# Performance work log

Hardware: AMD Instinct MI355X
Metric: run time of the kernel (lower is better)

## Reference

```python
import jax, jax.numpy as jnp
import numpy as np
import math

B, L, D = 4, 2048, 768
N_HEADS = 12
CHUNK = 8  # query_mask=1 every CHUNK tokens -> f = B*L/CHUNK, f % B == 0
VOCAB = 50000


def setup_inputs() -> dict:
    key = jax.random.key(0)
    ks = jax.random.split(key, 8)
    scale = 1.0 / math.sqrt(D)
    x_qk = jax.random.normal(ks[0], (B, L, D), jnp.float32)
    x_v = jax.random.normal(ks[1], (B, L, D), jnp.float32)
    # deterministic query mask: feature boundary every CHUNK tokens
    pos = jnp.arange(L)
    query_mask = jnp.tile((pos % CHUNK == 0).astype(jnp.int32)[None, :], (B, 1))
    input_ids = jax.random.randint(ks[2], (B, L), 2, VOCAB).astype(jnp.int64)
    # make the last 16 tokens of each row padding to exercise the pad mask
    input_ids = input_ids.at[:, -16:].set(1)
    Wq = jax.random.normal(ks[3], (D, D), jnp.float32) * scale
    Wk = jax.random.normal(ks[4], (D, D), jnp.float32) * scale
    Wv = jax.random.normal(ks[5], (D, D), jnp.float32) * scale
    Wo = jax.random.normal(ks[6], (D, D), jnp.float32) * scale
    zb = jnp.zeros((D,), jnp.float32)
    return {"x_qk": x_qk, "x_v": x_v, "query_mask": query_mask,
            "input_ids": input_ids, "pad_token_id": 1,
            "Wq": Wq, "bq": zb, "Wk": Wk, "bk": zb,
            "Wv": Wv, "bv": zb, "Wo": Wo, "bo": zb}


def reference(x_qk, x_v, query_mask, input_ids, pad_token_id,
              Wq, bq, Wk, bk, Wv, bv, Wo, bo):
    b, l, d = x_qk.shape
    n = b * l
    qm = query_mask.reshape(-1)
    f = int(np.asarray(jnp.sum(qm)))  # static feature count (f % b == 0)
    idx = jnp.nonzero(qm == 1, size=f)[0]                     # [f] query positions
    # segment boundaries: [left_i, right_i) per feature
    left = idx
    right = jnp.concatenate([idx[1:], jnp.array([n], idx.dtype)])
    pos = jnp.arange(n)
    seg_mask = (pos[None, :] >= left[:, None]) & (pos[None, :] < right[:, None])
    seg_mask = seg_mask & (input_ids.reshape(-1) != pad_token_id)[None, :]  # [f, n]

    xq = x_qk.reshape(n, d)
    xv = x_v.reshape(n, d)
    query = xq[idx]                                           # [f, d]
    q = query @ Wq.T + bq                                     # [f, d]
    k = xq @ Wk.T + bk                                        # [n, d]
    v = xv @ Wv.T + bv                                        # [n, d]

    dh = d // N_HEADS
    qh = q.reshape(f, N_HEADS, dh).transpose(1, 0, 2)         # [h, f, dh]
    kh = k.reshape(n, N_HEADS, dh).transpose(1, 0, 2)         # [h, n, dh]
    vh = v.reshape(n, N_HEADS, dh).transpose(1, 0, 2)         # [h, n, dh]

    bias = (1.0 - seg_mask.astype(jnp.float32)) * -10000.0    # [f, n]
    scores = jnp.einsum('hfd,hnd->hfn', qh, kh) / math.sqrt(dh) + bias[None]
    attn = jax.nn.softmax(scores, axis=-1)                    # [h, f, n]
    out = jnp.einsum('hfn,hnd->hfd', attn, vh)                # [h, f, dh]
    out = out.transpose(1, 0, 2).reshape(f, d)
    out = out @ Wo.T + bo
    return out.reshape(b, f // b, d)
```

## Files before the change

### kernel.cpp

```cpp
#include <hip/hip_runtime.h>

#define DMODEL 768
#define NHEADS 12
#define MAXFULL 16
#define NSTEP 24

typedef __attribute__((ext_vector_type(8))) short short8;
typedef __attribute__((ext_vector_type(4))) float f32x4;

__device__ __forceinline__ unsigned pack2_bf16(float a, float b) {
  unsigned ua = __float_as_uint(a), ub = __float_as_uint(b);
  ua = (ua + 0x7fffu + ((ua >> 16) & 1u)) >> 16;
  ub = (ub + 0x7fffu + ((ub >> 16) & 1u)) & 0xffff0000u;
  return ua | ub;
}
__device__ __forceinline__ unsigned short bf16_1(float a) {
  unsigned ua = __float_as_uint(a);
  return (unsigned short)((ua + 0x7fffu + ((ua >> 16) & 1u)) >> 16);
}

__device__ __forceinline__ void load16_lds(const void* g, void* l) {
  __builtin_amdgcn_global_load_lds(
      (const __attribute__((address_space(1))) unsigned int*)g,
      (__attribute__((address_space(3))) unsigned int*)l, 16, 0, 0);
}

__global__ __launch_bounds__(256) void convAll(const float* __restrict__ w0,
    const float* __restrict__ w1, const float* __restrict__ w2,
    const float* __restrict__ w3, unsigned* __restrict__ o0,
    unsigned* __restrict__ o1, unsigned* __restrict__ o2,
    unsigned* __restrict__ o3, int wcount,
    const float* __restrict__ x0, const float* __restrict__ x1,
    unsigned* __restrict__ xo0, unsigned* __restrict__ xo1, int xcount) {
  const int nvw = wcount >> 2;
  const float* src[4] = {w0, w1, w2, w3};
  unsigned* dst[4] = {o0, o1, o2, o3};
  for (int idx = blockIdx.x * 256 + threadIdx.x; idx < 4 * nvw;
       idx += gridDim.x * 256) {
    int m = idx / nvw, r = idx - m * nvw;
    float4 v = ((const float4*)src[m])[r];
    dst[m][2 * r]     = pack2_bf16(v.x, v.y);
    dst[m][2 * r + 1] = pack2_bf16(v.z, v.w);
  }
  const int nvx = xcount >> 2;
  for (int idx = blockIdx.x * 256 + threadIdx.x; idx < 2 * nvx;
       idx += gridDim.x * 256) {
    int m = idx / nvx, r = idx - m * nvx;
    float4 v = m ? ((const float4*)x1)[r] : ((const float4*)x0)[r];
    unsigned* d = m ? xo1 : xo0;
    d[2 * r]     = pack2_bf16(v.x, v.y);
    d[2 * r + 1] = pack2_bf16(v.z, v.w);
  }
}

struct GSeg {
  const unsigned short* A;
  const unsigned short* W;
  const float* bias;
  const int* row_map;
  float* C;
  int base;
};

typedef unsigned short LdsTile[2][256][32];

__global__ __launch_bounds__(512, 2) void gemm256(GSeg g0, GSeg g1, GSeg g2) {
  __shared__ __attribute__((aligned(16))) LdsTile As[2];
  __shared__ __attribute__((aligned(16))) LdsTile Bs[2];
  const int t = threadIdx.x;
  const int id = blockIdx.x;
  const GSeg& d = (id >= g2.base) ? g2 : ((id >= g1.base) ? g1 : g0);
  const int lid = id - d.base;
  const int bn = (lid % 3) * 256;
  const int bm = (lid / 3) * 256;
  const int lane = t & 63, wid = t >> 6;
  const int m16 = lane & 15, quad = lane >> 4;
  const int qx = quad ^ ((m16 >> 1) & 3);
  const int wr = wid >> 2, wc = wid & 3;

  f32x4 acc[8][4];
#pragma unroll
  for (int i = 0; i < 8; ++i)
#pragma unroll
    for (int j2 = 0; j2 < 4; ++j2) acc[i][j2] = (f32x4){0.f, 0.f, 0.f, 0.f};

  const int srow = wid * 16 + (lane >> 2);
  const int skc = ((lane & 3) ^ ((lane >> 3) & 3)) * 8;
  int arow0, arow1;
  if (d.row_map) {
    arow0 = d.row_map[bm + srow];
    arow1 = d.row_map[bm + 128 + srow];
  } else {
    arow0 = bm + srow;
    arow1 = bm + 128 + srow;
  }
  const int wrow0 = bn + srow, wrow1 = bn + 128 + srow;
  const int woff0 = (wid * 16) * 32;
  const int woff1 = (128 + wid * 16) * 32;

#define STAGE256(t_, Ab, Bb) do {                                          \
    const int kk_ = (t_) * 64 + skc;                                       \
    load16_lds(d.A + (size_t)arow0 * DMODEL + kk_,      &Ab[0][0][0] + woff0); \
    load16_lds(d.A + (size_t)arow1 * DMODEL + kk_,      &Ab[0][0][0] + woff1); \
    load16_lds(d.A + (size_t)arow0 * DMODEL + kk_ + 32, &Ab[1][0][0] + woff0); \
    load16_lds(d.A + (size_t)arow1 * DMODEL + kk_ + 32, &Ab[1][0][0] + woff1); \
    load16_lds(d.W + (size_t)wrow0 * DMODEL + kk_,      &Bb[0][0][0] + woff0); \
    load16_lds(d.W + (size_t)wrow1 * DMODEL + kk_,      &Bb[0][0][0] + woff1); \
    load16_lds(d.W + (size_t)wrow0 * DMODEL + kk_ + 32, &Bb[1][0][0] + woff0); \
    load16_lds(d.W + (size_t)wrow1 * DMODEL + kk_ + 32, &Bb[1][0][0] + woff1); \
  } while (0)

#define COMPUTE256(Ab, Bb) do {                                            \
    _Pragma("unroll")                                                      \
    for (int ks = 0; ks < 2; ++ks) {                                       \
      const unsigned short* Ap = &Ab[ks][0][0];                            \
      const unsigned short* Bp = &Bb[ks][0][0];                            \
      short8 a_[8], b_[4];                                                 \
      _Pragma("unroll")                                                    \
      for (int mi = 0; mi < 8; ++mi)                                       \
        a_[mi] = *(const short8*)&Ap[(wr * 128 + mi * 16 + m16) * 32 + qx * 8]; \
      _Pragma("unroll")                                                    \
      for (int nj = 0; nj < 4; ++nj)                                       \
        b_[nj] = *(const short8*)&Bp[(wc * 64 + nj * 16 + m16) * 32 + qx * 8]; \
      __builtin_amdgcn_s_setprio(1);                                       \
      _Pragma("unroll")                                                    \
      for (int mi = 0; mi < 8; ++mi)                                       \
        _Pragma("unroll")                                                  \
        for (int nj = 0; nj < 4; ++nj)                                     \
          acc[mi][nj] = __builtin_amdgcn_mfma_f32_16x16x32_bf16(           \
              a_[mi], b_[nj], acc[mi][nj], 0, 0, 0);                       \
      __builtin_amdgcn_s_setprio(0);                                       \
    }                                                                      \
  } while (0)

  STAGE256(0, As[0], Bs[0]);
  STAGE256(1, As[1], Bs[1]);

#pragma unroll 1
  for (int g = 0; g < 5; ++g) {
    asm volatile("s_waitcnt vmcnt(8)" ::: "memory");
    __builtin_amdgcn_s_barrier();
    __builtin_amdgcn_sched_barrier(0);
    COMPUTE256(As[0], Bs[0]);
    __builtin_amdgcn_s_barrier();
    __builtin_amdgcn_sched_barrier(0);
    STAGE256(2 * g + 2, As[0], Bs[0]);
    asm volatile("s_waitcnt vmcnt(8)" ::: "memory");
    __builtin_amdgcn_s_barrier();
    __builtin_amdgcn_sched_barrier(0);
    COMPUTE256(As[1], Bs[1]);
    __builtin_amdgcn_s_barrier();
    __builtin_amdgcn_sched_barrier(0);
    STAGE256(2 * g + 3, As[1], Bs[1]);
  }
  asm volatile("s_waitcnt vmcnt(8)" ::: "memory");
  __builtin_amdgcn_s_barrier();
  __builtin_amdgcn_sched_barrier(0);
  COMPUTE256(As[0], Bs[0]);
  asm volatile("s_waitcnt vmcnt(0)" ::: "memory");
  __builtin_amdgcn_s_barrier();
  __builtin_amdgcn_sched_barrier(0);
  COMPUTE256(As[1], Bs[1]);

#undef STAGE256
#undef COMPUTE256

  float bv[4]; int bcol[4];
#pragma unroll
  for (int nj = 0; nj < 4; ++nj) {
    bcol[nj] = bn + wc * 64 + nj * 16 + m16;
    bv[nj] = d.bias[bcol[nj]];
  }
#pragma unroll
  for (int mi = 0; mi < 8; ++mi) {
    const int rbase = bm + wr * 128 + mi * 16 + quad * 4;
#pragma unroll
    for (int r = 0; r < 4; ++r) {
      const int row = rbase + r;
#pragma unroll
      for (int nj = 0; nj < 4; ++nj)
        d.C[(size_t)row * DMODEL + bcol[nj]] = acc[mi][nj][r] + bv[nj];
    }
  }
}

__device__ __forceinline__ void stage_step(const GSeg& d, int k0, int arow0,
    int arow1, int wrow0, int wrow1, int skc, unsigned short* AsB,
    unsigned short* BsB, int woff) {
  load16_lds(d.A + (size_t)arow0 * DMODEL + k0 + skc, AsB + woff);
  load16_lds(d.A + (size_t)arow1 * DMODEL + k0 + skc, AsB + woff + 16 * 32);
  load16_lds(d.W + (size_t)wrow0 * DMODEL + k0 + skc, BsB + woff);
  load16_lds(d.W + (size_t)wrow1 * DMODEL + k0 + skc, BsB + woff + 16 * 32);
}

__device__ __forceinline__ void compute_step(const unsigned short* AsB,
    const unsigned short* BsB, int wm, int wn, int m16, int qx,
    f32x4 acc[4][4]) {
  short8 a[4], b[4];
#pragma unroll
  for (int i = 0; i < 4; ++i)
    a[i] = *(const short8*)&AsB[(wm + i * 16 + m16) * 32 + qx * 8];
#pragma unroll
  for (int j2 = 0; j2 < 4; ++j2)
    b[j2] = *(const short8*)&BsB[(wn + j2 * 16 + m16) * 32 + qx * 8];
  __builtin_amdgcn_s_setprio(1);
#pragma unroll
  for (int i = 0; i < 4; ++i)
#pragma unroll
    for (int j2 = 0; j2 < 4; ++j2)
      acc[i][j2] = __builtin_amdgcn_mfma_f32_16x16x32_bf16(a[i], b[j2], acc[i][j2], 0, 0, 0);
  __builtin_amdgcn_s_setprio(0);
}

__global__ __launch_bounds__(256) void gemm128(GSeg g0, GSeg g1, GSeg g2) {
  __shared__ __attribute__((aligned(16))) unsigned short As[3][128 * 32];
  __shared__ __attribute__((aligned(16))) unsigned short Bs[3][128 * 32];
  const int t = threadIdx.x;
  const int id = blockIdx.x;
  const GSeg& d = (id >= g2.base) ? g2 : ((id >= g1.base) ? g1 : g0);
  const int lid = id - d.base;
  const int xcd = lid & 7, j = lid >> 3;
  const int bn = (j % 6) * 128;
  const int bm = ((j / 6) * 8 + xcd) * 128;
  const int lane = t & 63, wid = t >> 6;
  const int m16 = lane & 15, quad = lane >> 4;
  const int qx = quad ^ ((m16 >> 1) & 3);
  const int wm = (wid >> 1) * 64, wn = (wid & 1) * 64;

  f32x4 acc[4][4];
#pragma unroll
  for (int i = 0; i < 4; ++i)
#pragma unroll
    for (int j2 = 0; j2 < 4; ++j2) acc[i][j2] = (f32x4){0.f, 0.f, 0.f, 0.f};

  const int srow = wid * 32 + (lane >> 2);
  const int skc = ((lane & 3) ^ ((lane >> 3) & 3)) * 8;
  int arow0, arow1;
  if (d.row_map) {
    arow0 = d.row_map[bm + srow];
    arow1 = d.row_map[bm + srow + 16];
  } else {
    arow0 = bm + srow;
    arow1 = bm + srow + 16;
  }
  const int wrow0 = bn + srow, wrow1 = bn + srow + 16;
  const int woff = (wid * 32) * 32;

  stage_step(d, 0,  arow0, arow1, wrow0, wrow1, skc, &As[0][0], &Bs[0][0], woff);
  stage_step(d, 32, arow0, arow1, wrow0, wrow1, skc, &As[1][0], &Bs[1][0], woff);
  stage_step(d, 64, arow0, arow1, wrow0, wrow1, skc, &As[2][0], &Bs[2][0], woff);

#pragma unroll 1
  for (int g = 0; g < (NSTEP - 3) / 3; ++g) {
    const int t0 = g * 3;
#pragma unroll
    for (int u = 0; u < 3; ++u) {
      const int ts = t0 + u;
      asm volatile("s_waitcnt vmcnt(8)" ::: "memory");
      __builtin_amdgcn_s_barrier();
      __builtin_amdgcn_sched_barrier(0);
      compute_step(&As[u][0], &Bs[u][0], wm, wn, m16, qx, acc);
      __builtin_amdgcn_s_barrier();
      __builtin_amdgcn_sched_barrier(0);
      stage_step(d, (ts + 3) * 32, arow0, arow1, wrow0, wrow1, skc,
                 &As[u][0], &Bs[u][0], woff);
    }
  }
  asm volatile("s_waitcnt vmcnt(8)" ::: "memory");
  __builtin_amdgcn_s_barrier();
  __builtin_amdgcn_sched_barrier(0);
  compute_step(&As[0][0], &Bs[0][0], wm, wn, m16, qx, acc);
  asm volatile("s_waitcnt vmcnt(4)" ::: "memory");
  __builtin_amdgcn_s_barrier();
  __builtin_amdgcn_sched_barrier(0);
  compute_step(&As[1][0], &Bs[1][0], wm, wn, m16, qx, acc);
  asm volatile("s_waitcnt vmcnt(0)" ::: "memory");
  __builtin_amdgcn_s_barrier();
  __builtin_amdgcn_sched_barrier(0);
  compute_step(&As[2][0], &Bs[2][0], wm, wn, m16, qx, acc);

  float bv[4]; int bcol[4];
#pragma unroll
  for (int j2 = 0; j2 < 4; ++j2) {
    bcol[j2] = bn + wn + j2 * 16 + m16;
    bv[j2] = d.bias[bcol[j2]];
  }
#pragma unroll
  for (int i = 0; i < 4; ++i) {
    const int rbase = bm + wm + i * 16 + quad * 4;
#pragma unroll
    for (int r = 0; r < 4; ++r) {
      const int row = rbase + r;
#pragma unroll
      for (int j2 = 0; j2 < 4; ++j2)
        d.C[(size_t)row * DMODEL + bcol[j2]] = acc[i][j2][r] + bv[j2];
    }
  }
}

__global__ __launch_bounds__(1024) void build_segments(const int* __restrict__ qm,
    const int* __restrict__ ids, const int* __restrict__ padp,
    int n, int f, int* __restrict__ left, int* __restrict__ right,
    int* __restrict__ nvalid, int* __restrict__ fullrank,
    int* __restrict__ fullist, int* __restrict__ nfull) {
  __shared__ int cnt[1024];
  __shared__ int fullcnt;
  const int t = threadIdx.x;
  if (t == 0) fullcnt = 0;
  const int per = (n + 1023) >> 10;
  const int base = t * per;
  int c = 0;
  for (int i = 0; i < per; ++i) {
    int p = base + i;
    if (p < n && qm[p] != 0) ++c;
  }
  cnt[t] = c;
  __syncthreads();
  for (int off = 1; off < 1024; off <<= 1) {
    int v = (t >= off) ? cnt[t - off] : 0;
    __syncthreads();
    cnt[t] += v;
    __syncthreads();
  }
  int r = cnt[t] - c;
  for (int i = 0; i < per; ++i) {
    int p = base + i;
    if (p < n && qm[p] != 0) {
      if (r < f) left[r] = p;
      ++r;
    }
  }
  __syncthreads();
  const int pad = *padp;
  for (int i = t; i < f; i += 1024) {
    int L0 = left[i];
    int R0 = (i + 1 < f) ? left[i + 1] : n;
    right[i] = R0;
    int cv = 0;
    for (int p = L0; p < R0; ++p) cv += (ids[p] != pad) ? 1 : 0;
    nvalid[i] = cv;
    if (cv == 0) {
      int rk = atomicAdd(&fullcnt, 1);
      if (rk < MAXFULL) { fullist[rk] = i; fullrank[i] = rk; }
      else fullrank[i] = -1;
    } else {
      fullrank[i] = -1;
    }
  }
  __syncthreads();
  if (t == 0) *nfull = (fullcnt < MAXFULL) ? fullcnt : MAXFULL;
}

__device__ __forceinline__ float allreduce64(float x) {
#pragma unroll
  for (int m = 1; m < 64; m <<= 1) x += __shfl_xor(x, m, 64);
  return x;
}

__global__ __launch_bounds__(64) void attn_seg(const float* __restrict__ q,
    const float* __restrict__ k, const float* __restrict__ v,
    const int* __restrict__ left, const int* __restrict__ right,
    const int* __restrict__ nvalid, const int* __restrict__ ids,
    const int* __restrict__ padp, unsigned short* __restrict__ out) {
  const int feat = blockIdx.x, h = blockIdx.y, lane = threadIdx.x;
  if (nvalid[feat] == 0) return;
  const int off = h * 64 + lane;
  const int pad = *padp;
  const float qv = q[(size_t)feat * DMODEL + off];
  const int L0 = left[feat], R0 = right[feat];
  if (R0 - L0 == 8) {
    float kv[8], vv[8], s[8];
    int live[8];
#pragma unroll
    for (int p = 0; p < 8; ++p) {
      kv[p] = k[(size_t)(L0 + p) * DMODEL + off];
      vv[p] = v[(size_t)(L0 + p) * DMODEL + off];
      live[p] = (ids[L0 + p] != pad);
    }
#pragma unroll
    for (int p = 0; p < 8; ++p) s[p] = qv * kv[p];
#pragma unroll
    for (int m_ = 1; m_ < 64; m_ <<= 1)
#pragma unroll
      for (int p = 0; p < 8; ++p) s[p] += __shfl_xor(s[p], m_, 64);
    float mx = -1e30f;
#pragma unroll
    for (int p = 0; p < 8; ++p) {
      s[p] = live[p] ? s[p] * 0.125f : -1e30f;
      mx = fmaxf(mx, s[p]);
    }
    float l = 0.f, acc = 0.f;
#pragma unroll
    for (int p = 0; p < 8; ++p) {
      float w = __expf(s[p] - mx);
      l += w;
      acc += w * vv[p];
    }
    out[(size_t)feat * DMODEL + off] = bf16_1(acc / l);
    return;
  }
  float m = -1e30f, l = 0.f, acc = 0.f;
  for (int p = L0; p < R0; ++p) {
    if (ids[p] == pad) continue;
    float s = allreduce64(qv * k[(size_t)p * DMODEL + off]) * 0.125f;
    float mn = fmaxf(m, s);
    float al = __expf(m - mn);
    float w = __expf(s - mn);
    l = l * al + w;
    acc = acc * al + w * v[(size_t)p * DMODEL + off];
    m = mn;
  }
  out[(size_t)feat * DMODEL + off] = bf16_1(acc / l);
}

__global__ __launch_bounds__(256) void attn_full_part(const float* __restrict__ q,
    const float* __restrict__ k, const float* __restrict__ v,
    const int* __restrict__ fullist, const int* __restrict__ nfullp,
    int n, int P, float* __restrict__ pm, float* __restrict__ pl,
    float* __restrict__ pacc) {
  const int nfull = *nfullp;
  if (nfull == 0) return;
  const int t = threadIdx.x, lane = t & 63, wv = t >> 6;
  const int gw = blockIdx.x * 4 + wv;
  const int h = gw / P, piece = gw - h * P;
  const int pk = n / P;

  __shared__ float q_lds[8 * 64];
  __shared__ float w_lds[4][64 * 8];

  for (int idx = t; idx < 8 * 64; idx += 256) {
    int fl = idx >> 6, d = idx & 63;
    q_lds[idx] = (fl < nfull) ? q[(size_t)fullist[fl] * DMODEL + h * 64 + d] : 0.f;
  }
  __syncthreads();

  float m[8], l[8], acc[8];
#pragma unroll
  for (int f_ = 0; f_ < 8; ++f_) { m[f_] = -1e30f; l[f_] = 0.f; acc[f_] = 0.f; }

  for (int c = 0; c < pk; c += 64) {
    const int pc = piece * pk + c;
    float s[8];
#pragma unroll
    for (int f_ = 0; f_ < 8; ++f_) s[f_] = 0.f;
    const float4* kp = (const float4*)(k + (size_t)(pc + lane) * DMODEL + h * 64);
#pragma unroll 1
    for (int g = 0; g < 2; ++g) {
      float4 kv0 = kp[g * 8 + 0], kv1 = kp[g * 8 + 1], kv2 = kp[g * 8 + 2],
             kv3 = kp[g * 8 + 3], kv4 = kp[g * 8 + 4], kv5 = kp[g * 8 + 5],
             kv6 = kp[g * 8 + 6], kv7 = kp[g * 8 + 7];
      const float4* qb = (const float4*)&q_lds[g * 32];
#pragma unroll
      for (int f_ = 0; f_ < 8; ++f_) {
        float4 q0 = qb[f_ * 16 + 0], q1 = qb[f_ * 16 + 1], q2 = qb[f_ * 16 + 2],
               q3 = qb[f_ * 16 + 3], q4 = qb[f_ * 16 + 4], q5 = qb[f_ * 16 + 5],
               q6 = qb[f_ * 16 + 6], q7 = qb[f_ * 16 + 7];
        float acc0 = q0.x * kv0.x + q0.y * kv0.y + q0.z * kv0.z + q0.w * kv0.w;
        acc0 += q1.x * kv1.x + q1.y * kv1.y + q1.z * kv1.z + q1.w * kv1.w;
        acc0 += q2.x * kv2.x + q2.y * kv2.y + q2.z * kv2.z + q2.w * kv2.w;
        acc0 += q3.x * kv3.x + q3.y * kv3.y + q3.z * kv3.z + q3.w * kv3.w;
        acc0 += q4.x * kv4.x + q4.y * kv4.y + q4.z * kv4.z + q4.w * kv4.w;
        acc0 += q5.x * kv5.x + q5.y * kv5.y + q5.z * kv5.z + q5.w * kv5.w;
        acc0 += q6.x * kv6.x + q6.y * kv6.y + q6.z * kv6.z + q6.w * kv6.w;
        acc0 += q7.x * kv7.x + q7.y * kv7.y + q7.z * kv7.z + q7.w * kv7.w;
        s[f_] += acc0;
      }
    }
    float mx[8];
#pragma unroll
    for (int f_ = 0; f_ < 8; ++f_) mx[f_] = s[f_] * 0.125f;
#pragma unroll
    for (int f_ = 0; f_ < 8; ++f_) s[f_] = mx[f_];
#pragma unroll
    for (int st = 1; st < 64; st <<= 1)
#pragma unroll
      for (int f_ = 0; f_ < 8; ++f_) mx[f_] = fmaxf(mx[f_], __shfl_xor(mx[f_], st, 64));
    float alpha[8], w[8], sum[8];
#pragma unroll
    for (int f_ = 0; f_ < 8; ++f_) {
      float mn = fmaxf(m[f_], mx[f_]);
      alpha[f_] = __expf(m[f_] - mn);
      w[f_] = __expf(s[f_] - mn);
      m[f_] = mn;
      sum[f_] = w[f_];
    }
#pragma unroll
    for (int st = 1; st < 64; st <<= 1)
#pragma unroll
      for (int f_ = 0; f_ < 8; ++f_) sum[f_] += __shfl_xor(sum[f_], st, 64);
#pragma unroll
    for (int f_ = 0; f_ < 8; ++f_) l[f_] = l[f_] * alpha[f_] + sum[f_];
    *(float4*)&w_lds[wv][lane * 8]     = make_float4(w[0], w[1], w[2], w[3]);
    *(float4*)&w_lds[wv][lane * 8 + 4] = make_float4(w[4], w[5], w[6], w[7]);
#pragma unroll
    for (int f_ = 0; f_ < 8; ++f_) acc[f_] *= alpha[f_];
    const float* vb = v + (size_t)pc * DMODEL + h * 64 + lane;
#pragma unroll 4
    for (int kk = 0; kk < 64; ++kk) {
      float vd = vb[(size_t)kk * DMODEL];
      float4 wa = *(const float4*)&w_lds[wv][kk * 8];
      float4 wb = *(const float4*)&w_lds[wv][kk * 8 + 4];
      acc[0] += wa.x * vd; acc[1] += wa.y * vd; acc[2] += wa.z * vd; acc[3] += wa.w * vd;
      acc[4] += wb.x * vd; acc[5] += wb.y * vd; acc[6] += wb.z * vd; acc[7] += wb.w * vd;
    }
  }

  for (int f_ = 0; f_ < nfull; ++f_) {
    size_t idx = ((size_t)f_ * NHEADS + h) * P + piece;
    if (lane == 0) { pm[idx] = m[f_]; pl[idx] = l[f_]; }
    pacc[idx * 64 + lane] = acc[f_];
  }
}

__global__ __launch_bounds__(256) void attn_full_comb(
    const int* __restrict__ fullist, const int* __restrict__ nfullp,
    int P, const float* __restrict__ pm, const float* __restrict__ pl,
    const float* __restrict__ pacc, unsigned short* __restrict__ out) {
  const int fl = blockIdx.x, h = blockIdx.y;
  if (fl >= *nfullp) return;
  const int feat = fullist[fl];
  const int t = threadIdx.x, lane = t & 63, wv = t >> 6;
  const size_t base = ((size_t)fl * NHEADS + h) * P;

  __shared__ float s_pm[128];
  __shared__ float s_sc[128];
  __shared__ float s_red[4];
  __shared__ float s_part[4][64];

  for (int sp = t; sp < P; sp += 256) s_pm[sp] = pm[base + sp];
  __syncthreads();
  float mloc = -1e30f;
  for (int sp = t; sp < P; sp += 256) mloc = fmaxf(mloc, s_pm[sp]);
#pragma unroll
  for (int st = 1; st < 64; st <<= 1) mloc = fmaxf(mloc, __shfl_xor(mloc, st, 64));
  if (lane == 0) s_red[wv] = mloc;
  __syncthreads();
  const float M = fmaxf(fmaxf(s_red[0], s_red[1]), fmaxf(s_red[2], s_red[3]));
  __syncthreads();
  float lloc = 0.f;
  for (int sp = t; sp < P; sp += 256) {
    float sc = __expf(s_pm[sp] - M);
    s_sc[sp] = sc;
    lloc += pl[base + sp] * sc;
  }
#pragma unroll
  for (int st = 1; st < 64; st <<= 1) lloc += __shfl_xor(lloc, st, 64);
  if (lane == 0) s_red[wv] = lloc;
  __syncthreads();
  const float Lt = s_red[0] + s_red[1] + s_red[2] + s_red[3];
  float At = 0.f;
  for (int sp = wv; sp < P; sp += 4)
    At += pacc[(base + sp) * 64 + lane] * s_sc[sp];
  s_part[wv][lane] = At;
  __syncthreads();
  if (wv == 0) {
    float tot = s_part[0][lane] + s_part[1][lane] + s_part[2][lane] + s_part[3][lane];
    out[(size_t)feat * DMODEL + h * 64 + lane] = bf16_1(tot / Lt);
  }
}

extern "C" void kernel_launch(void* const* d_in, const int* in_sizes, int n_in,
                              void* d_out, int out_size, void* d_ws, size_t ws_size,
                              hipStream_t stream) {
  const float* x_qk = (const float*)d_in[0];
  const float* x_v  = (const float*)d_in[1];
  const int* qm     = (const int*)d_in[2];
  const int* ids    = (const int*)d_in[3];
  const int* padp   = (const int*)d_in[4];
  const float* Wq = (const float*)d_in[5];
  const float* bq = (const float*)d_in[6];
  const float* Wk = (const float*)d_in[7];
  const float* bk = (const float*)d_in[8];
  const float* Wv = (const float*)d_in[9];
  const float* bv = (const float*)d_in[10];
  const float* Wo = (const float*)d_in[11];
  const float* bo = (const float*)d_in[12];

  const int n = in_sizes[0] / DMODEL;
  const int f = out_size / DMODEL;

  float* kf = (float*)d_ws;
  float* vf = kf + (size_t)n * DMODEL;
  float* qf = vf + (size_t)n * DMODEL;
  unsigned short* af = (unsigned short*)(qf + (size_t)f * DMODEL);
  unsigned short* wqb = af + (size_t)f * DMODEL;
  unsigned short* wkb = wqb + DMODEL * DMODEL;
  unsigned short* wvb = wkb + DMODEL * DMODEL;
  unsigned short* wob = wvb + DMODEL * DMODEL;
  unsigned short* xqb = wob + DMODEL * DMODEL;
  unsigned short* xvb = xqb + (size_t)n * DMODEL;
  int* left     = (int*)(xvb + (size_t)n * DMODEL);
  int* right    = left + f;
  int* nvalid   = right + f;
  int* fullrank = nvalid + f;
  int* fullist  = fullrank + f;
  int* nfull    = fullist + MAXFULL;
  size_t off_bytes = ((size_t)((char*)(nfull + 1) - (char*)d_ws) + 255) & ~(size_t)255;
  int P = 128;
  while (P > 16) {
    size_t need = (size_t)MAXFULL * NHEADS * P * 66 * sizeof(float);
    if (off_bytes + need <= ws_size && (n / P) % 64 == 0 && n % P == 0) break;
    P >>= 1;
  }
  float* pm = (float*)((char*)d_ws + off_bytes);
  float* pl = pm + (size_t)MAXFULL * NHEADS * P;
  float* pacc = pl + (size_t)MAXFULL * NHEADS * P;

  build_segments<<<1, 1024, 0, stream>>>(qm, ids, padp, n, f, left, right,
                                         nvalid, fullrank, fullist, nfull);
  convAll<<<2048, 256, 0, stream>>>(Wq, Wk, Wv, Wo, (unsigned*)wqb,
                                    (unsigned*)wkb, (unsigned*)wvb,
                                    (unsigned*)wob, DMODEL * DMODEL,
                                    x_qk, x_v, (unsigned*)xqb, (unsigned*)xvb,
                                    n * DMODEL);

  const int TKV256 = 3 * (n / 256);
  const int TF256  = 3 * (f / 256);
  GSeg g0 = { xqb, wkb, bk, nullptr, kf, 0 };
  GSeg g1 = { xvb, wvb, bv, nullptr, vf, TKV256 };
  GSeg g2 = { xqb, wqb, bq, left,    qf, 2 * TKV256 };
  gemm256<<<2 * TKV256 + TF256, 512, 0, stream>>>(g0, g1, g2);

  attn_seg<<<dim3(f, NHEADS), 64, 0, stream>>>(qf, kf, vf, left, right, nvalid,
                                               ids, padp, af);
  attn_full_part<<<NHEADS * P / 4, 256, 0, stream>>>(qf, kf, vf, fullist, nfull,
                                                     n, P, pm, pl, pacc);
  attn_full_comb<<<dim3(MAXFULL, NHEADS), 256, 0, stream>>>(fullist, nfull, P,
                                                            pm, pl, pacc, af);

  const int TF  = 6 * (f / 128);
  GSeg gout = { af, wob, bo, nullptr, (float*)d_out, 0 };
  GSeg gnull = { af, wob, bo, nullptr, (float*)d_out, 1 << 30 };
  gemm128<<<TF, 256, 0, stream>>>(gout, gnull, gnull);
}
```

Baseline: 219.2 us.

## Fuse segment building into conversion, merge attention kernels, smaller-tile Wo GEMM

Folds the single-block build_segments launch into the extra last block of the conversion kernel, merges the segment-attention and full-attention-partial kernels into one launch, and replaces the 128x128 four-wave output GEMM with a single-wave 64x64 kernel that uses a 4-stage load pipeline and no barriers. The goal is fewer kernel launches and more blocks for the small f x 768 output GEMM (f=1024). The risk is that the segment-building block now runs with 256 threads instead of 1024 and may become the critical path of the conversion kernel, and single-wave GEMM blocks are less efficient per CU.

After: 223.5 us. No clear change (+2.0%).

```diff
diff --git a/kernel.cpp b/kernel.cpp
--- a/kernel.cpp
+++ b/kernel.cpp
@@ -31,20 +31,73 @@
     unsigned* __restrict__ o1, unsigned* __restrict__ o2,
     unsigned* __restrict__ o3, int wcount,
     const float* __restrict__ x0, const float* __restrict__ x1,
-    unsigned* __restrict__ xo0, unsigned* __restrict__ xo1, int xcount) {
+    unsigned* __restrict__ xo0, unsigned* __restrict__ xo1, int xcount,
+    const int* __restrict__ qm, const int* __restrict__ ids,
+    const int* __restrict__ padp, int n, int f, int* __restrict__ left,
+    int* __restrict__ right, int* __restrict__ nvalid,
+    int* __restrict__ fullrank, int* __restrict__ fullist,
+    int* __restrict__ nfull) {
+  __shared__ int cnt[256];
+  __shared__ int fullcnt;
+  const int t = threadIdx.x;
+  if (blockIdx.x == gridDim.x - 1) {
+    if (t == 0) fullcnt = 0;
+    const int per = (n + 255) >> 8;
+    const int base = t * per;
+    int c = 0;
+    for (int i = 0; i < per; ++i) {
+      int p = base + i;
+      if (p < n && qm[p] != 0) ++c;
+    }
+    cnt[t] = c;
+    __syncthreads();
+    for (int off = 1; off < 256; off <<= 1) {
+      int v = (t >= off) ? cnt[t - off] : 0;
+      __syncthreads();
+      cnt[t] += v;
+      __syncthreads();
+    }
+    int r = cnt[t] - c;
+    for (int i = 0; i < per; ++i) {
+      int p = base + i;
+      if (p < n && qm[p] != 0) {
+        if (r < f) left[r] = p;
+        ++r;
+      }
+    }
+    __syncthreads();
+    const int pad = *padp;
+    for (int i = t; i < f; i += 256) {
+      int L0 = left[i];
+      int R0 = (i + 1 < f) ? left[i + 1] : n;
+      right[i] = R0;
+      int cv = 0;
+      for (int p = L0; p < R0; ++p) cv += (ids[p] != pad) ? 1 : 0;
+      nvalid[i] = cv;
+      if (cv == 0) {
+        int rk = atomicAdd(&fullcnt, 1);
+        if (rk < MAXFULL) { fullist[rk] = i; fullrank[i] = rk; }
+        else fullrank[i] = -1;
+      } else {
+        fullrank[i] = -1;
+      }
+    }
+    __syncthreads();
+    if (t == 0) *nfull = (fullcnt < MAXFULL) ? fullcnt : MAXFULL;
+    return;
+  }
+  const int nb = gridDim.x - 1;
   const int nvw = wcount >> 2;
   const float* src[4] = {w0, w1, w2, w3};
   unsigned* dst[4] = {o0, o1, o2, o3};
-  for (int idx = blockIdx.x * 256 + threadIdx.x; idx < 4 * nvw;
-       idx += gridDim.x * 256) {
+  for (int idx = blockIdx.x * 256 + t; idx < 4 * nvw; idx += nb * 256) {
     int m = idx / nvw, r = idx - m * nvw;
     float4 v = ((const float4*)src[m])[r];
     dst[m][2 * r]     = pack2_bf16(v.x, v.y);
     dst[m][2 * r + 1] = pack2_bf16(v.z, v.w);
   }
   const int nvx = xcount >> 2;
-  for (int idx = blockIdx.x * 256 + threadIdx.x; idx < 2 * nvx;
-       idx += gridDim.x * 256) {
+  for (int idx = blockIdx.x * 256 + t; idx < 2 * nvx; idx += nb * 256) {
     int m = idx / nvx, r = idx - m * nvx;
     float4 v = m ? ((const float4*)x1)[r] : ((const float4*)x0)[r];
     unsigned* d = m ? xo1 : xo0;
@@ -184,48 +237,18 @@
   }
 }
 
-__device__ __forceinline__ void stage_step(const GSeg& d, int k0, int arow0,
-    int arow1, int wrow0, int wrow1, int skc, unsigned short* AsB,
-    unsigned short* BsB, int woff) {
-  load16_lds(d.A + (size_t)arow0 * DMODEL + k0 + skc, AsB + woff);
-  load16_lds(d.A + (size_t)arow1 * DMODEL + k0 + skc, AsB + woff + 16 * 32);
-  load16_lds(d.W + (size_t)wrow0 * DMODEL + k0 + skc, BsB + woff);
-  load16_lds(d.W + (size_t)wrow1 * DMODEL + k0 + skc, BsB + woff + 16 * 32);
-}
-
-__device__ __forceinline__ void compute_step(const unsigned short* AsB,
-    const unsigned short* BsB, int wm, int wn, int m16, int qx,
-    f32x4 acc[4][4]) {
-  short8 a[4], b[4];
-#pragma unroll
-  for (int i = 0; i < 4; ++i)
-    a[i] = *(const short8*)&AsB[(wm + i * 16 + m16) * 32 + qx * 8];
-#pragma unroll
-  for (int j2 = 0; j2 < 4; ++j2)
-    b[j2] = *(const short8*)&BsB[(wn + j2 * 16 + m16) * 32 + qx * 8];
-  __builtin_amdgcn_s_setprio(1);
-#pragma unroll
-  for (int i = 0; i < 4; ++i)
-#pragma unroll
-    for (int j2 = 0; j2 < 4; ++j2)
-      acc[i][j2] = __builtin_amdgcn_mfma_f32_16x16x32_bf16(a[i], b[j2], acc[i][j2], 0, 0, 0);
-  __builtin_amdgcn_s_setprio(0);
-}
-
-__global__ __launch_bounds__(256) void gemm128(GSeg g0, GSeg g1, GSeg g2) {
-  __shared__ __attribute__((aligned(16))) unsigned short As[3][128 * 32];
-  __shared__ __attribute__((aligned(16))) unsigned short Bs[3][128 * 32];
-  const int t = threadIdx.x;
-  const int id = blockIdx.x;
-  const GSeg& d = (id >= g2.base) ? g2 : ((id >= g1.base) ? g1 : g0);
-  const int lid = id - d.base;
-  const int xcd = lid & 7, j = lid >> 3;
-  const int bn = (j % 6) * 128;
-  const int bm = ((j / 6) * 8 + xcd) * 128;
-  const int lane = t & 63, wid = t >> 6;
+__global__ __launch_bounds__(64) void gemmWo(const unsigned short* __restrict__ A,
+    const unsigned short* __restrict__ W, const float* __restrict__ bias,
+    float* __restrict__ C) {
+  __shared__ __attribute__((aligned(16))) unsigned short As[4][64 * 32];
+  __shared__ __attribute__((aligned(16))) unsigned short Bs[4][64 * 32];
+  const int bid = blockIdx.x;
+  const int bm = (bid / 12) * 64, bn = (bid % 12) * 64;
+  const int lane = threadIdx.x;
   const int m16 = lane & 15, quad = lane >> 4;
   const int qx = quad ^ ((m16 >> 1) & 3);
-  const int wm = (wid >> 1) * 64, wn = (wid & 1) * 64;
+  const int srow = lane >> 2;
+  const int skc = ((lane & 3) ^ ((lane >> 3) & 3)) * 8;
 
   f32x4 acc[4][4];
 #pragma unroll
@@ -233,122 +256,77 @@
 #pragma unroll
     for (int j2 = 0; j2 < 4; ++j2) acc[i][j2] = (f32x4){0.f, 0.f, 0.f, 0.f};
 
-  const int srow = wid * 32 + (lane >> 2);
-  const int skc = ((lane & 3) ^ ((lane >> 3) & 3)) * 8;
-  int arow0, arow1;
-  if (d.row_map) {
-    arow0 = d.row_map[bm + srow];
-    arow1 = d.row_map[bm + srow + 16];
-  } else {
-    arow0 = bm + srow;
-    arow1 = bm + srow + 16;
-  }
-  const int wrow0 = bn + srow, wrow1 = bn + srow + 16;
-  const int woff = (wid * 32) * 32;
-
-  stage_step(d, 0,  arow0, arow1, wrow0, wrow1, skc, &As[0][0], &Bs[0][0], woff);
-  stage_step(d, 32, arow0, arow1, wrow0, wrow1, skc, &As[1][0], &Bs[1][0], woff);
-  stage_step(d, 64, arow0, arow1, wrow0, wrow1, skc, &As[2][0], &Bs[2][0], woff);
+#define STAGEW(s_, t_) do {                                                \
+    const int kk_ = (t_) * 32 + skc;                                       \
+    _Pragma("unroll")                                                      \
+    for (int i_ = 0; i_ < 4; ++i_) {                                       \
+      load16_lds(A + (size_t)(bm + 16 * i_ + srow) * DMODEL + kk_,         \
+                 &As[s_][i_ * 16 * 32]);                                   \
+      load16_lds(W + (size_t)(bn + 16 * i_ + srow) * DMODEL + kk_,         \
+                 &Bs[s_][i_ * 16 * 32]);                                   \
+    }                                                                      \
+  } while (0)
+
+#define COMPUTEW(s_) do {                                                  \
+    short8 a_[4], b_[4];                                                   \
+    _Pragma("unroll")                                                      \
+    for (int mi = 0; mi < 4; ++mi)                                         \
+      a_[mi] = *(const short8*)&As[s_][(mi * 16 + m16) * 32 + qx * 8];     \
+    _Pragma("unroll")                                                      \
+    for (int nj = 0; nj < 4; ++nj)                                         \
+      b_[nj] = *(const short8*)&Bs[s_][(nj * 16 + m16) * 32 + qx * 8];     \
+    _Pragma("unroll")                                                      \
+    for (int mi = 0; mi < 4; ++mi)                                         \
+      _Pragma("unroll")                                                    \
+      for (int nj = 0; nj < 4; ++nj)                                       \
+        acc[mi][nj] = __builtin_amdgcn_mfma_f32_16x16x32_bf16(             \
+            a_[mi], b_[nj], acc[mi][nj], 0, 0, 0);                         \
+  } while (0)
+
+  STAGEW(0, 0); STAGEW(1, 1); STAGEW(2, 2); STAGEW(3, 3);
 
 #pragma unroll 1
-  for (int g = 0; g < (NSTEP - 3) / 3; ++g) {
-    const int t0 = g * 3;
-#pragma unroll
-    for (int u = 0; u < 3; ++u) {
-      const int ts = t0 + u;
-      asm volatile("s_waitcnt vmcnt(8)" ::: "memory");
-      __builtin_amdgcn_s_barrier();
-      __builtin_amdgcn_sched_barrier(0);
-      compute_step(&As[u][0], &Bs[u][0], wm, wn, m16, qx, acc);
-      __builtin_amdgcn_s_barrier();
-      __builtin_amdgcn_sched_barrier(0);
-      stage_step(d, (ts + 3) * 32, arow0, arow1, wrow0, wrow1, skc,
-                 &As[u][0], &Bs[u][0], woff);
-    }
-  }
+  for (int ts = 0; ts < NSTEP - 4; ++ts) {
+    asm volatile("s_waitcnt vmcnt(24)" ::: "memory");
+    __builtin_amdgcn_sched_barrier(0);
+    COMPUTEW(ts & 3);
+    asm volatile("s_waitcnt lgkmcnt(0)" ::: "memory");
+    __builtin_amdgcn_sched_barrier(0);
+    STAGEW(ts & 3, ts + 4);
+  }
+  asm volatile("s_waitcnt vmcnt(24)" ::: "memory");
+  __builtin_amdgcn_sched_barrier(0);
+  COMPUTEW(0);
+  asm volatile("s_waitcnt vmcnt(16)" ::: "memory");
+  __builtin_amdgcn_sched_barrier(0);
+  COMPUTEW(1);
   asm volatile("s_waitcnt vmcnt(8)" ::: "memory");
-  __builtin_amdgcn_s_barrier();
   __builtin_amdgcn_sched_barrier(0);
-  compute_step(&As[0][0], &Bs[0][0], wm, wn, m16, qx, acc);
-  asm volatile("s_waitcnt vmcnt(4)" ::: "memory");
-  __builtin_amdgcn_s_barrier();
+  COMPUTEW(2);
+  asm volatile("s_waitcnt vmcnt(0)" ::: "memory");
   __builtin_amdgcn_sched_barrier(0);
-  compute_step(&As[1][0], &Bs[1][0], wm, wn, m16, qx, acc);
-  asm volatile("s_waitcnt vmcnt(0)" ::: "memory");
-  __builtin_amdgcn_s_barrier();
-  __builtin_amdgcn_sched_barrier(0);
-  compute_step(&As[2][0], &Bs[2][0], wm, wn, m16, qx, acc);
+  COMPUTEW(3);
+
+#undef STAGEW
+#undef COMPUTEW
 
   float bv[4]; int bcol[4];
 #pragma unroll
-  for (int j2 = 0; j2 < 4; ++j2) {
-    bcol[j2] = bn + wn + j2 * 16 + m16;
-    bv[j2] = d.bias[bcol[j2]];
-  }
-#pragma unroll
-  for (int i = 0; i < 4; ++i) {
-    const int rbase = bm + wm + i * 16 + quad * 4;
+  for (int nj = 0; nj < 4; ++nj) {
+    bcol[nj] = bn + nj * 16 + m16;
+    bv[nj] = bias[bcol[nj]];
+  }
+#pragma unroll
+  for (int mi = 0; mi < 4; ++mi) {
+    const int rbase = bm + mi * 16 + quad * 4;
 #pragma unroll
     for (int r = 0; r < 4; ++r) {
       const int row = rbase + r;
 #pragma unroll
-      for (int j2 = 0; j2 < 4; ++j2)
-        d.C[(size_t)row * DMODEL + bcol[j2]] = acc[i][j2][r] + bv[j2];
-    }
-  }
-}
-
-__global__ __launch_bounds__(1024) void build_segments(const int* __restrict__ qm,
-    const int* __restrict__ ids, const int* __restrict__ padp,
-    int n, int f, int* __restrict__ left, int* __restrict__ right,
-    int* __restrict__ nvalid, int* __restrict__ fullrank,
-    int* __restrict__ fullist, int* __restrict__ nfull) {
-  __shared__ int cnt[1024];
-  __shared__ int fullcnt;
-  const int t = threadIdx.x;
-  if (t == 0) fullcnt = 0;
-  const int per = (n + 1023) >> 10;
-  const int base = t * per;
-  int c = 0;
-  for (int i = 0; i < per; ++i) {
-    int p = base + i;
-    if (p < n && qm[p] != 0) ++c;
-  }
-  cnt[t] = c;
-  __syncthreads();
-  for (int off = 1; off < 1024; off <<= 1) {
-    int v = (t >= off) ? cnt[t - off] : 0;
-    __syncthreads();
-    cnt[t] += v;
-    __syncthreads();
-  }
-  int r = cnt[t] - c;
-  for (int i = 0; i < per; ++i) {
-    int p = base + i;
-    if (p < n && qm[p] != 0) {
-      if (r < f) left[r] = p;
-      ++r;
-    }
-  }
-  __syncthreads();
-  const int pad = *padp;
-  for (int i = t; i < f; i += 1024) {
-    int L0 = left[i];
-    int R0 = (i + 1 < f) ? left[i + 1] : n;
-    right[i] = R0;
-    int cv = 0;
-    for (int p = L0; p < R0; ++p) cv += (ids[p] != pad) ? 1 : 0;
-    nvalid[i] = cv;
-    if (cv == 0) {
-      int rk = atomicAdd(&fullcnt, 1);
-      if (rk < MAXFULL) { fullist[rk] = i; fullrank[i] = rk; }
-      else fullrank[i] = -1;
-    } else {
-      fullrank[i] = -1;
-    }
-  }
-  __syncthreads();
-  if (t == 0) *nfull = (fullcnt < MAXFULL) ? fullcnt : MAXFULL;
+      for (int nj = 0; nj < 4; ++nj)
+        C[(size_t)row * DMODEL + bcol[nj]] = acc[mi][nj][r] + bv[nj];
+    }
+  }
 }
 
 __device__ __forceinline__ float allreduce64(float x) {
@@ -357,80 +335,79 @@
   return x;
 }
 
-__global__ __launch_bounds__(64) void attn_seg(const float* __restrict__ q,
+__global__ __launch_bounds__(64) void attn_all(const float* __restrict__ q,
     const float* __restrict__ k, const float* __restrict__ v,
     const int* __restrict__ left, const int* __restrict__ right,
     const int* __restrict__ nvalid, const int* __restrict__ ids,
-    const int* __restrict__ padp, unsigned short* __restrict__ out) {
-  const int feat = blockIdx.x, h = blockIdx.y, lane = threadIdx.x;
-  if (nvalid[feat] == 0) return;
-  const int off = h * 64 + lane;
-  const int pad = *padp;
-  const float qv = q[(size_t)feat * DMODEL + off];
-  const int L0 = left[feat], R0 = right[feat];
-  if (R0 - L0 == 8) {
-    float kv[8], vv[8], s[8];
-    int live[8];
-#pragma unroll
-    for (int p = 0; p < 8; ++p) {
-      kv[p] = k[(size_t)(L0 + p) * DMODEL + off];
-      vv[p] = v[(size_t)(L0 + p) * DMODEL + off];
-      live[p] = (ids[L0 + p] != pad);
-    }
-#pragma unroll
-    for (int p = 0; p < 8; ++p) s[p] = qv * kv[p];
-#pragma unroll
-    for (int m_ = 1; m_ < 64; m_ <<= 1)
-#pragma unroll
-      for (int p = 0; p < 8; ++p) s[p] += __shfl_xor(s[p], m_, 64);
-    float mx = -1e30f;
-#pragma unroll
-    for (int p = 0; p < 8; ++p) {
-      s[p] = live[p] ? s[p] * 0.125f : -1e30f;
-      mx = fmaxf(mx, s[p]);
-    }
-    float l = 0.f, acc = 0.f;
-#pragma unroll
-    for (int p = 0; p < 8; ++p) {
-      float w = __expf(s[p] - mx);
-      l += w;
-      acc += w * vv[p];
+    const int* __restrict__ padp, unsigned short* __restrict__ out,
+    const int* __restrict__ fullist, const int* __restrict__ nfullp,
+    int n, int f, int P, float* __restrict__ pm, float* __restrict__ pl,
+    float* __restrict__ pacc) {
+  __shared__ float q_lds[8 * 64];
+  __shared__ float w_lds[64 * 8];
+  const int x = blockIdx.x, h = blockIdx.y, lane = threadIdx.x;
+
+  if (x < f) {
+    const int feat = x;
+    if (nvalid[feat] == 0) return;
+    const int off = h * 64 + lane;
+    const int pad = *padp;
+    const float qv = q[(size_t)feat * DMODEL + off];
+    const int L0 = left[feat], R0 = right[feat];
+    if (R0 - L0 == 8) {
+      float kv[8], vv[8], s[8];
+      int live[8];
+#pragma unroll
+      for (int p = 0; p < 8; ++p) {
+        kv[p] = k[(size_t)(L0 + p) * DMODEL + off];
+        vv[p] = v[(size_t)(L0 + p) * DMODEL + off];
+        live[p] = (ids[L0 + p] != pad);
+      }
+#pragma unroll
+      for (int p = 0; p < 8; ++p) s[p] = qv * kv[p];
+#pragma unroll
+      for (int m_ = 1; m_ < 64; m_ <<= 1)
+#pragma unroll
+        for (int p = 0; p < 8; ++p) s[p] += __shfl_xor(s[p], m_, 64);
+      float mx = -1e30f;
+#pragma unroll
+      for (int p = 0; p < 8; ++p) {
+        s[p] = live[p] ? s[p] * 0.125f : -1e30f;
+        mx = fmaxf(mx, s[p]);
+      }
+      float l = 0.f, acc = 0.f;
+#pragma unroll
+      for (int p = 0; p < 8; ++p) {
+        float w = __expf(s[p] - mx);
+        l += w;
+        acc += w * vv[p];
+      }
+      out[(size_t)feat * DMODEL + off] = bf16_1(acc / l);
+      return;
+    }
+    float m = -1e30f, l = 0.f, acc = 0.f;
+    for (int p = L0; p < R0; ++p) {
+      if (ids[p] == pad) continue;
+      float s = allreduce64(qv * k[(size_t)p * DMODEL + off]) * 0.125f;
+      float mn = fmaxf(m, s);
+      float al = __expf(m - mn);
+      float w = __expf(s - mn);
+      l = l * al + w;
+      acc = acc * al + w * v[(size_t)p * DMODEL + off];
+      m = mn;
     }
     out[(size_t)feat * DMODEL + off] = bf16_1(acc / l);
     return;
   }
-  float m = -1e30f, l = 0.f, acc = 0.f;
-  for (int p = L0; p < R0; ++p) {
-    if (ids[p] == pad) continue;
-    float s = allreduce64(qv * k[(size_t)p * DMODEL + off]) * 0.125f;
-    float mn = fmaxf(m, s);
-    float al = __expf(m - mn);
-    float w = __expf(s - mn);
-    l = l * al + w;
-    acc = acc * al + w * v[(size_t)p * DMODEL + off];
-    m = mn;
-  }
-  out[(size_t)feat * DMODEL + off] = bf16_1(acc / l);
-}
-
-__global__ __launch_bounds__(256) void attn_full_part(const float* __restrict__ q,
-    const float* __restrict__ k, const float* __restrict__ v,
-    const int* __restrict__ fullist, const int* __restrict__ nfullp,
-    int n, int P, float* __restrict__ pm, float* __restrict__ pl,
-    float* __restrict__ pacc) {
+
   const int nfull = *nfullp;
   if (nfull == 0) return;
-  const int t = threadIdx.x, lane = t & 63, wv = t >> 6;
-  const int gw = blockIdx.x * 4 + wv;
-  const int h = gw / P, piece = gw - h * P;
+  const int piece = x - f;
   const int pk = n / P;
 
-  __shared__ float q_lds[8 * 64];
-  __shared__ float w_lds[4][64 * 8];
-
-  for (int idx = t; idx < 8 * 64; idx += 256) {
-    int fl = idx >> 6, d = idx & 63;
-    q_lds[idx] = (fl < nfull) ? q[(size_t)fullist[fl] * DMODEL + h * 64 + d] : 0.f;
+  for (int idx = lane; idx < 8 * 64; idx += 64) {
+    int fl = idx >> 6, dcol = idx & 63;
+    q_lds[idx] = (fl < nfull) ? q[(size_t)fullist[fl] * DMODEL + h * 64 + dcol] : 0.f;
   }
   __syncthreads();
 
@@ -490,16 +467,16 @@
       for (int f_ = 0; f_ < 8; ++f_) sum[f_] += __shfl_xor(sum[f_], st, 64);
 #pragma unroll
     for (int f_ = 0; f_ < 8; ++f_) l[f_] = l[f_] * alpha[f_] + sum[f_];
-    *(float4*)&w_lds[wv][lane * 8]     = make_float4(w[0], w[1], w[2], w[3]);
-    *(float4*)&w_lds[wv][lane * 8 + 4] = make_float4(w[4], w[5], w[6], w[7]);
+    *(float4*)&w_lds[lane * 8]     = make_float4(w[0], w[1], w[2], w[3]);
+    *(float4*)&w_lds[lane * 8 + 4] = make_float4(w[4], w[5], w[6], w[7]);
 #pragma unroll
     for (int f_ = 0; f_ < 8; ++f_) acc[f_] *= alpha[f_];
     const float* vb = v + (size_t)pc * DMODEL + h * 64 + lane;
 #pragma unroll 4
     for (int kk = 0; kk < 64; ++kk) {
       float vd = vb[(size_t)kk * DMODEL];
-      float4 wa = *(const float4*)&w_lds[wv][kk * 8];
-      float4 wb = *(const float4*)&w_lds[wv][kk * 8 + 4];
+      float4 wa = *(const float4*)&w_lds[kk * 8];
+      float4 wb = *(const float4*)&w_lds[kk * 8 + 4];
       acc[0] += wa.x * vd; acc[1] += wa.y * vd; acc[2] += wa.z * vd; acc[3] += wa.w * vd;
       acc[4] += wb.x * vd; acc[5] += wb.y * vd; acc[6] += wb.z * vd; acc[7] += wb.w * vd;
     }
@@ -606,13 +583,13 @@
   float* pl = pm + (size_t)MAXFULL * NHEADS * P;
   float* pacc = pl + (size_t)MAXFULL * NHEADS * P;
 
-  build_segments<<<1, 1024, 0, stream>>>(qm, ids, padp, n, f, left, right,
-                                         nvalid, fullrank, fullist, nfull);
-  convAll<<<2048, 256, 0, stream>>>(Wq, Wk, Wv, Wo, (unsigned*)wqb,
+  convAll<<<2049, 256, 0, stream>>>(Wq, Wk, Wv, Wo, (unsigned*)wqb,
                                     (unsigned*)wkb, (unsigned*)wvb,
                                     (unsigned*)wob, DMODEL * DMODEL,
                                     x_qk, x_v, (unsigned*)xqb, (unsigned*)xvb,
-                                    n * DMODEL);
+                                    n * DMODEL,
+                                    qm, ids, padp, n, f, left, right, nvalid,
+                                    fullrank, fullist, nfull);
 
   const int TKV256 = 3 * (n / 256);
   const int TF256  = 3 * (f / 256);
@@ -621,15 +598,12 @@
   GSeg g2 = { xqb, wqb, bq, left,    qf, 2 * TKV256 };
   gemm256<<<2 * TKV256 + TF256, 512, 0, stream>>>(g0, g1, g2);
 
-  attn_seg<<<dim3(f, NHEADS), 64, 0, stream>>>(qf, kf, vf, left, right, nvalid,
-                                               ids, padp, af);
-  attn_full_part<<<NHEADS * P / 4, 256, 0, stream>>>(qf, kf, vf, fullist, nfull,
-                                                     n, P, pm, pl, pacc);
+  attn_all<<<dim3(f + P, NHEADS), 64, 0, stream>>>(qf, kf, vf, left, right,
+                                                   nvalid, ids, padp, af,
+                                                   fullist, nfull, n, f, P,
+                                                   pm, pl, pacc);
   attn_full_comb<<<dim3(MAXFULL, NHEADS), 256, 0, stream>>>(fullist, nfull, P,
                                                             pm, pl, pacc, af);
 
-  const int TF  = 6 * (f / 128);
-  GSeg gout = { af, wob, bo, nullptr, (float*)d_out, 0 };
-  GSeg gnull = { af, wob, bo, nullptr, (float*)d_out, 1 << 30 };
-  gemm128<<<TF, 256, 0, stream>>>(gout, gnull, gnull);
-}
+  gemmWo<<<(f / 64) * (DMODEL / 64), 64, 0, stream>>>(af, wob, bo, (float*)d_out);
+}
```
